# Kernel tuning notes

Measured on AMD Instinct MI355X. Metric: run time of the kernel, lower is better.

The kernel has to match this reference:

```python
import jax, jax.numpy as jnp
import numpy as np

N_BITS = 8
QMAX = 2 ** N_BITS - 1


def fake_quant(x, axis=None):
    """Min-max asymmetric uniform fake quantization with STE.
    axis=None -> per-tensor; axis=i -> per-channel along dim i."""
    if axis is None:
        mn = jnp.min(x)
        mx = jnp.max(x)
    else:
        red = tuple(i for i in range(x.ndim) if i != axis % x.ndim)
        mn = jnp.min(x, axis=red, keepdims=True)
        mx = jnp.max(x, axis=red, keepdims=True)
    mn = jnp.minimum(mn, 0.0)
    mx = jnp.maximum(mx, 0.0)
    scale = jnp.maximum((mx - mn) / QMAX, 1e-8)
    zp = jnp.round(-mn / scale)
    q = jnp.clip(jnp.round(x / scale) + zp, 0.0, QMAX)
    dq = (q - zp) * scale
    return x + jax.lax.stop_gradient(dq - x)


def setup_inputs() -> dict:
    key = jax.random.key(0)
    ks = jax.random.split(key, 5)
    B, N, C = 32, 577, 1024
    return {
        "x": jax.random.normal(ks[0], (B, N, C), dtype=jnp.float32),
        "qkv_w": jax.random.normal(ks[1], (3 * C, C), dtype=jnp.float32) * 0.02,
        "qkv_b": jax.random.normal(ks[2], (3 * C,), dtype=jnp.float32) * 0.02,
        "proj_w": jax.random.normal(ks[3], (C, C), dtype=jnp.float32) * 0.02,
        "proj_b": jax.random.normal(ks[4], (C,), dtype=jnp.float32) * 0.02,
    }


def reference(x, qkv_w, qkv_b, proj_w, proj_b):
    B, N, C = x.shape
    H = 16
    D = C // H
    scale = 1.0 / jnp.sqrt(jnp.float32(D))  # 0.125

    # QuantLinear qkv: per-channel act quant (channel_wise=True), per-out-channel weight quant
    xq = fake_quant(x, axis=-1)
    wq = fake_quant(qkv_w, axis=0)
    qkv = xq @ wq.T + qkv_b                       # [B,N,3C]
    qkv = qkv.reshape(B, N, 3, H, D).transpose(2, 0, 3, 1, 4)  # [3,B,H,N,D]
    q, k, v = qkv[0], qkv[1], qkv[2]

    # QuantMatMul 1: quantize both q and k^T (per-tensor)
    attn = jnp.einsum('bhnd,bhmd->bhnm', fake_quant(q), fake_quant(k)) * scale
    attn = jax.nn.softmax(attn, axis=-1)

    # QuantMatMul 2: disable_quantizer_a -> attn NOT quantized, only v
    out = jnp.einsum('bhnm,bhmd->bhnd', attn, fake_quant(v))  # [B,H,N,D]
    out = out.transpose(0, 2, 1, 3).reshape(B, N, C)

    # QuantLinear proj: per-tensor act quant, per-out-channel weight quant
    oq = fake_quant(out)
    pw = fake_quant(proj_w, axis=0)
    return oq @ pw.T + proj_b
```

## Files before the change

### kernel.cpp

```cpp
#include <hip/hip_runtime.h>

typedef unsigned short u16;
typedef float f32x4 __attribute__((ext_vector_type(4)));
typedef u16 u16x8 __attribute__((ext_vector_type(8)));
typedef u16 u16x4 __attribute__((ext_vector_type(4)));
typedef __bf16 bf16x8 __attribute__((ext_vector_type(8)));

#define M_ROWS 18464
#define NSEQ   577
#define NPAD   608
#define QMAXF  255.0f

static constexpr size_t OFF_IX  = 0;
static constexpr size_t OFF_BH  = 37814272;
static constexpr size_t OFF_BL  = 44105728;
static constexpr size_t OFF_IK  = 0;
static constexpr size_t OFF_IO  = 0;
static constexpr size_t OFF_F32 = 50397184;
static constexpr size_t OFF_IQ  = 50397184;
static constexpr size_t OFF_IVT = 126025728;
static constexpr size_t OFF_IPW = 165871616;
static constexpr size_t OFF_PAR = 167968768;
static constexpr size_t WS_NEED = 168100000;

#define P_XMN   0
#define P_XMX   1024
#define P_SX    2048
#define P_ZPX   3072
#define P_SWQ   4096
#define P_SPW   7168
#define P_QKVMM 8192
#define P_OUTMM 8198
#define P_PQ    8200
#define P_PO    8208

__device__ __forceinline__ u16 f2bf(float f){
  unsigned u = __float_as_uint(f);
  unsigned r = u + 0x7fffu + ((u >> 16) & 1u);
  return (u16)(r >> 16);
}
__device__ __forceinline__ float bf2f(u16 h){ return __uint_as_float(((unsigned)h) << 16); }

__device__ __forceinline__ unsigned ford(float f){
  unsigned u = __float_as_uint(f);
  return (u & 0x80000000u) ? ~u : (u | 0x80000000u);
}
__device__ __forceinline__ float unford(unsigned u){
  return (u & 0x80000000u) ? __uint_as_float(u & 0x7fffffffu) : __uint_as_float(~u);
}

__device__ __forceinline__ f32x4 mfma16(u16x8 a, u16x8 b, f32x4 c){
  return __builtin_amdgcn_mfma_f32_16x16x32_bf16(
      __builtin_bit_cast(bf16x8, a), __builtin_bit_cast(bf16x8, b), c, 0, 0, 0);
}

__device__ __forceinline__ void gload_lds16(const void* g, void* l){
  __builtin_amdgcn_global_load_lds((const __attribute__((address_space(1))) unsigned int*)g,
                                   (__attribute__((address_space(3))) unsigned int*)l,
                                   16, 0, 0);
}

__device__ __forceinline__ void tilemap(int id, int nwg, int NT, int GM, int& mt, int& nt){
  int q = nwg >> 3;
  int swz = (id & 7) * q + (id >> 3);
  int gsz = GM * NT;
  int g = swz / gsz, r = swz % gsz;
  mt = g * GM + (r % GM);
  nt = r / GM;
}

__global__ void k_init(unsigned* par){
  int t = threadIdx.x;
  for (int i = t; i < 1024; i += 256){ par[P_XMN + i] = 0xFFFFFFFFu; par[P_XMX + i] = 0u; }
  if (t < 6) par[P_QKVMM + t] = (t & 1) ? 0u : 0xFFFFFFFFu;
  if (t < 2) par[P_OUTMM + t] = (t & 1) ? 0u : 0xFFFFFFFFu;
}

__global__ void k_minmax_x(const float* __restrict__ x, unsigned* par){
  int t = threadIdx.x;
  int r0 = blockIdx.x * 145;
  int r1 = min(r0 + 145, M_ROWS);
  float mn[4], mx[4];
#pragma unroll
  for (int e = 0; e < 4; e++){ mn[e] = 1e38f; mx[e] = -1e38f; }
  for (int r = r0; r < r1; r++){
    f32x4 v = *(const f32x4*)&x[(size_t)r * 1024 + t * 4];
#pragma unroll
    for (int e = 0; e < 4; e++){ mn[e] = fminf(mn[e], v[e]); mx[e] = fmaxf(mx[e], v[e]); }
  }
#pragma unroll
  for (int e = 0; e < 4; e++){
    atomicMin(&par[P_XMN + t * 4 + e], ford(mn[e]));
    atomicMax(&par[P_XMX + t * 4 + e], ford(mx[e]));
  }
}

__global__ void k_params_x(unsigned* paru){
  float* par = (float*)paru;
  int c = blockIdx.x * 256 + threadIdx.x;
  if (c < 1024){
    float mn = unford(paru[P_XMN + c]);
    float mx = unford(paru[P_XMX + c]);
    mn = fminf(mn, 0.f); mx = fmaxf(mx, 0.f);
    float s = fmaxf((mx - mn) / QMAXF, 1e-8f);
    par[P_SX + c] = s;
    par[P_ZPX + c] = rintf(-mn / s);
  }
}

__global__ void k_quant_x(const float* __restrict__ x, const float* __restrict__ par, u16* __restrict__ ix){
  const int total = M_ROWS * 1024 / 4;
  for (int i = blockIdx.x * blockDim.x + threadIdx.x; i < total; i += gridDim.x * blockDim.x){
    f32x4 v  = *(const f32x4*)&x[(size_t)i * 4];
    int c = (i * 4) & 1023;
    f32x4 s  = *(const f32x4*)&par[P_SX + c];
    f32x4 zp = *(const f32x4*)&par[P_ZPX + c];
    u16x4 o;
#pragma unroll
    for (int e = 0; e < 4; e++){
      float q = fminf(fmaxf(rintf(v[e] / s[e]) + zp[e], 0.f), QMAXF);
      o[e] = f2bf(q - zp[e]);
    }
    *(u16x4*)&ix[(size_t)i * 4] = o;
  }
}

__global__ void k_quant_wqkv(const float* __restrict__ w, const float* __restrict__ par,
                             float* __restrict__ swq, u16* __restrict__ Bh, u16* __restrict__ Bl){
  int lane = threadIdx.x & 63, wv = threadIdx.x >> 6;
  int row = blockIdx.x * 4 + wv;
  const float* wr = w + (size_t)row * 1024;
  f32x4 v[4];
  float mn = 1e38f, mx = -1e38f;
#pragma unroll
  for (int j = 0; j < 4; j++){
    v[j] = *(const f32x4*)&wr[j * 256 + lane * 4];
#pragma unroll
    for (int e = 0; e < 4; e++){ mn = fminf(mn, v[j][e]); mx = fmaxf(mx, v[j][e]); }
  }
#pragma unroll
  for (int m = 1; m < 64; m <<= 1){ mn = fminf(mn, __shfl_xor(mn, m)); mx = fmaxf(mx, __shfl_xor(mx, m)); }
  mn = fminf(mn, 0.f); mx = fmaxf(mx, 0.f);
  float s = fmaxf((mx - mn) / QMAXF, 1e-8f);
  float zp = rintf(-mn / s);
  if (lane == 0) swq[row] = s;
#pragma unroll
  for (int j = 0; j < 4; j++){
    int c = j * 256 + lane * 4;
    f32x4 sx = *(const f32x4*)&par[P_SX + c];
    u16x4 oh, ol;
#pragma unroll
    for (int e = 0; e < 4; e++){
      float q = fminf(fmaxf(rintf(v[j][e] / s) + zp, 0.f), QMAXF);
      float bp = sx[e] * (q - zp);
      u16 hh = f2bf(bp);
      oh[e] = hh;
      ol[e] = f2bf(bp - bf2f(hh));
    }
    *(u16x4*)&Bh[(size_t)row * 1024 + c] = oh;
    *(u16x4*)&Bl[(size_t)row * 1024 + c] = ol;
  }
}

__global__ void k_quant_wproj(const float* __restrict__ w, float* __restrict__ spw, u16* __restrict__ ipw){
  int lane = threadIdx.x & 63, wv = threadIdx.x >> 6;
  int row = blockIdx.x * 4 + wv;
  const float* wr = w + (size_t)row * 1024;
  f32x4 v[4];
  float mn = 1e38f, mx = -1e38f;
#pragma unroll
  for (int j = 0; j < 4; j++){
    v[j] = *(const f32x4*)&wr[j * 256 + lane * 4];
#pragma unroll
    for (int e = 0; e < 4; e++){ mn = fminf(mn, v[j][e]); mx = fmaxf(mx, v[j][e]); }
  }
#pragma unroll
  for (int m = 1; m < 64; m <<= 1){ mn = fminf(mn, __shfl_xor(mn, m)); mx = fmaxf(mx, __shfl_xor(mx, m)); }
  mn = fminf(mn, 0.f); mx = fmaxf(mx, 0.f);
  float s = fmaxf((mx - mn) / QMAXF, 1e-8f);
  float zp = rintf(-mn / s);
  if (lane == 0) spw[row] = s;
#pragma unroll
  for (int j = 0; j < 4; j++){
    int c = j * 256 + lane * 4;
    u16x4 o;
#pragma unroll
    for (int e = 0; e < 4; e++){
      float q = fminf(fmaxf(rintf(v[j][e] / s) + zp, 0.f), QMAXF);
      o[e] = f2bf(q - zp);
    }
    *(u16x4*)&ipw[(size_t)row * 1024 + c] = o;
  }
}

__global__ __launch_bounds__(256) void k_gemm_qkvpart(const u16* __restrict__ A,
    const u16* __restrict__ Bh, const u16* __restrict__ Bl, const float* __restrict__ swq,
    const float* __restrict__ bias, int bcol_off, int NT, float* dst0, float* dst1,
    int seg0, unsigned* paru){
  __shared__ u16 As[128 * 32], Bhs[128 * 32], Bls[128 * 32];
  int tid = threadIdx.x, lane = tid & 63, w = tid >> 6;
  int mt, nt; tilemap(blockIdx.x, gridDim.x, NT, 29, mt, nt);
  int m0 = mt * 128, n0 = nt * 128;
  int wr = (w >> 1) * 64, wc = (w & 1) * 64;
  f32x4 zero = {0.f, 0.f, 0.f, 0.f};
  f32x4 acc[4][4];
#pragma unroll
  for (int m = 0; m < 4; m++)
#pragma unroll
    for (int n = 0; n < 4; n++) acc[m][n] = zero;
  int kc = (lane & 3) * 8;
  for (int kt = 0; kt < 1024; kt += 32){
    __syncthreads();
#pragma unroll
    for (int i = 0; i < 2; i++){
      int ci = w * 2 + i;
      int r = ci * 16 + (lane >> 2);
      int gra = min(m0 + r, M_ROWS - 1);
      gload_lds16(&A[(size_t)gra * 1024 + kt + kc], &As[ci * 512]);
      size_t grb = (size_t)(bcol_off + n0 + r) * 1024 + kt + kc;
      gload_lds16(&Bh[grb], &Bhs[ci * 512]);
      gload_lds16(&Bl[grb], &Bls[ci * 512]);
    }
    __syncthreads();
    u16x8 af[4];
#pragma unroll
    for (int m = 0; m < 4; m++)
      af[m] = *(const u16x8*)&As[(wr + m * 16 + (lane & 15)) * 32 + (lane >> 4) * 8];
#pragma unroll
    for (int n = 0; n < 4; n++){
      u16x8 bh = *(const u16x8*)&Bhs[(wc + n * 16 + (lane & 15)) * 32 + (lane >> 4) * 8];
      u16x8 bl = *(const u16x8*)&Bls[(wc + n * 16 + (lane & 15)) * 32 + (lane >> 4) * 8];
#pragma unroll
      for (int m = 0; m < 4; m++){
        acc[m][n] = mfma16(af[m], bh, acc[m][n]);
        acc[m][n] = mfma16(af[m], bl, acc[m][n]);
      }
    }
  }
  float lmn = 1e38f, lmx = -1e38f;
#pragma unroll
  for (int n = 0; n < 4; n++){
    int cl = n0 + wc + n * 16 + (lane & 15);
    float sw = swq[bcol_off + cl], bv = bias[bcol_off + cl];
    float* dst = (cl < 1024) ? dst0 : dst1;
    int cs = cl & 1023;
#pragma unroll
    for (int m = 0; m < 4; m++){
      int rb = m0 + wr + m * 16 + (lane >> 4) * 4;
#pragma unroll
      for (int j = 0; j < 4; j++){
        int row = rb + j;
        if (row < M_ROWS){
          float vv = acc[m][n][j] * sw + bv;
          dst[(size_t)row * 1024 + cs] = vv;
          lmn = fminf(lmn, vv); lmx = fmaxf(lmx, vv);
        }
      }
    }
  }
  int seg = seg0 + (n0 >> 10);
#pragma unroll
  for (int m = 32; m; m >>= 1){ lmn = fminf(lmn, __shfl_xor(lmn, m)); lmx = fmaxf(lmx, __shfl_xor(lmx, m)); }
  if (lane == 0){
    atomicMin(&paru[P_QKVMM + seg * 2], ford(lmn));
    atomicMax(&paru[P_QKVMM + seg * 2 + 1], ford(lmx));
  }
}

__global__ void k_params_v(unsigned* paru){
  if (threadIdx.x == 0){
    float* par = (float*)paru;
    float mn = unford(paru[P_QKVMM + 4]);
    float mx = unford(paru[P_QKVMM + 5]);
    mn = fminf(mn, 0.f); mx = fmaxf(mx, 0.f);
    float s = fmaxf((mx - mn) / QMAXF, 1e-8f);
    par[P_PQ + 4] = s;
    par[P_PQ + 5] = rintf(-mn / s);
  }
}

__global__ void k_params_qk(unsigned* paru){
  if (threadIdx.x == 0){
    float* par = (float*)paru;
    float sv[2];
    for (int t = 0; t < 2; t++){
      float mn = unford(paru[P_QKVMM + t * 2]);
      float mx = unford(paru[P_QKVMM + t * 2 + 1]);
      mn = fminf(mn, 0.f); mx = fmaxf(mx, 0.f);
      float s = fmaxf((mx - mn) / QMAXF, 1e-8f);
      sv[t] = s;
      par[P_PQ + t * 2] = s;
      par[P_PQ + t * 2 + 1] = rintf(-mn / s);
    }
    par[P_PQ + 6] = sv[0] * sv[1] * 0.125f;
  }
}

__global__ void k_quant_v(const float* __restrict__ vbuf, const float* __restrict__ par,
                          u16* __restrict__ ivT){
  int bh = blockIdx.x, b = bh >> 4, h = bh & 15;
  int tid = threadIdx.x;
  __shared__ unsigned vtu[64][37];
  float s = par[P_PQ + 4], zp = par[P_PQ + 5];
  const float* vsrc = vbuf + (size_t)b * 577 * 1024 + h * 64;
  u16* vdst = ivT + (size_t)bh * 64 * NPAD;
  for (int c0 = 0; c0 < 10; c0++){
    int n0 = c0 * 64;
    __syncthreads();
    for (int idx = tid; idx < 64 * 32; idx += 256){
      int d = idx & 63, p = idx >> 6;
      int n1 = n0 + 2 * p, n2 = n1 + 1;
      float v1 = 0.f, v2 = 0.f;
      if (n1 < NSEQ){
        float xx = vsrc[(size_t)n1 * 1024 + d];
        float q = fminf(fmaxf(rintf(xx / s) + zp, 0.f), QMAXF);
        v1 = q - zp;
      }
      if (n2 < NSEQ){
        float xx = vsrc[(size_t)n2 * 1024 + d];
        float q = fminf(fmaxf(rintf(xx / s) + zp, 0.f), QMAXF);
        v2 = q - zp;
      }
      vtu[d][p] = (unsigned)f2bf(v1) | ((unsigned)f2bf(v2) << 16);
    }
    __syncthreads();
    for (int idx = tid; idx < 64 * 32; idx += 256){
      int p = idx & 31, d = idx >> 5;
      int n = n0 + 2 * p;
      if (n < NPAD) *(unsigned*)&vdst[(size_t)d * NPAD + n] = vtu[d][p];
    }
  }
}

__global__ void k_quant_nd(const float* __restrict__ buf, const float* __restrict__ par,
                           int pidx, u16* __restrict__ dst){
  int bh = blockIdx.x, b = bh >> 4, h = bh & 15;
  int tid = threadIdx.x;
  float s = par[P_PQ + pidx], zp = par[P_PQ + pidx + 1];
  u16* d0p = dst + (size_t)bh * NPAD * 64;
  for (int idx = tid; idx < NPAD * 16; idx += 256){
    int n = idx >> 4, d0 = (idx & 15) * 4;
    u16x4 o = {0, 0, 0, 0};
    if (n < NSEQ){
      f32x4 v = *(const f32x4*)&buf[((size_t)(b * 577 + n)) * 1024 + h * 64 + d0];
#pragma unroll
      for (int e = 0; e < 4; e++){
        float q = fminf(fmaxf(rintf(v[e] / s) + zp, 0.f), QMAXF);
        o[e] = f2bf(q - zp);
      }
    }
    *(u16x4*)&d0p[n * 64 + d0] = o;
  }
}

__global__ __launch_bounds__(256) void k_attn(const u16* __restrict__ iq, const u16* __restrict__ ik,
    const u16* __restrict__ ivT, const float* __restrict__ par, float* __restrict__ out, unsigned* paru){
  __shared__ __attribute__((aligned(16))) u16 plds[4][2][2][16][40];
  int tile = blockIdx.x;
  int xcd = tile & 7, slot = tile >> 3;
  int bh = (slot / 5) * 8 + xcd, qt = slot % 5;
  int b = bh >> 4, h = bh & 15;
  int tid = threadIdx.x, lane = tid & 63, w = tid >> 6;
  int lo = lane & 15, hi = lane >> 4;
  int q0 = qt * 128 + w * 32;
  const u16* iqp = iq + (size_t)bh * NPAD * 64;
  const u16* ikp = ik + (size_t)bh * NPAD * 64;
  const u16* ivp = ivT + (size_t)bh * 64 * NPAD;
  float lscale = par[P_PQ + 6];
  u16x8 qf[2][2];
#pragma unroll
  for (int g = 0; g < 2; g++){
    int qr = min(q0 + g * 16 + lo, NPAD - 1);
#pragma unroll
    for (int ks = 0; ks < 2; ks++)
      qf[g][ks] = *(const u16x8*)&iqp[(size_t)qr * 64 + ks * 32 + hi * 8];
  }
  f32x4 zero = {0.f, 0.f, 0.f, 0.f};
  f32x4 oacc[2][4];
  float mrow[2][4], lrow[2][4];
#pragma unroll
  for (int g = 0; g < 2; g++){
#pragma unroll
    for (int n = 0; n < 4; n++) oacc[g][n] = zero;
#pragma unroll
    for (int j = 0; j < 4; j++){ mrow[g][j] = -1e30f; lrow[g][j] = 0.f; }
  }
  for (int kt = 0; kt < 19; kt++){
    int k0 = kt * 32;
    u16x8 vf[4];
#pragma unroll
    for (int n = 0; n < 4; n++)
      vf[n] = *(const u16x8*)&ivp[(size_t)(n * 16 + lo) * NPAD + k0 + hi * 8];
    u16x8 kf[2][2];
#pragma unroll
    for (int t = 0; t < 2; t++)
#pragma unroll
      for (int ks = 0; ks < 2; ks++)
        kf[t][ks] = *(const u16x8*)&ikp[(size_t)(k0 + t * 16 + lo) * 64 + ks * 32 + hi * 8];
    f32x4 acc[2][2];
#pragma unroll
    for (int g = 0; g < 2; g++)
#pragma unroll
      for (int t = 0; t < 2; t++){
        f32x4 a = mfma16(qf[g][0], kf[t][0], zero);
        acc[g][t] = mfma16(qf[g][1], kf[t][1], a);
      }
    int kg0 = k0 + lo;
#pragma unroll
    for (int g = 0; g < 2; g++){
#pragma unroll
      for (int j = 0; j < 4; j++){
        float s0 = (kg0 < NSEQ) ? acc[g][0][j] * lscale : -1e30f;
        float s1 = (kg0 + 16 < NSEQ) ? acc[g][1][j] * lscale : -1e30f;
        float mx = fmaxf(s0, s1);
#pragma unroll
        for (int mk = 1; mk < 16; mk <<= 1) mx = fmaxf(mx, __shfl_xor(mx, mk));
        float mnew = fmaxf(mrow[g][j], mx);
        float sf = __expf(mrow[g][j] - mnew);
        mrow[g][j] = mnew;
        float p0 = __expf(s0 - mnew);
        float p1 = __expf(s1 - mnew);
        float ps = p0 + p1;
#pragma unroll
        for (int mk = 1; mk < 16; mk <<= 1) ps += __shfl_xor(ps, mk);
        lrow[g][j] = lrow[g][j] * sf + ps;
#pragma unroll
        for (int n = 0; n < 4; n++) oacc[g][n][j] *= sf;
        int row = hi * 4 + j;
        u16 h0 = f2bf(p0), h1 = f2bf(p1);
        plds[w][g][0][row][lo]      = h0;
        plds[w][g][0][row][lo + 16] = h1;
        plds[w][g][1][row][lo]      = f2bf(p0 - bf2f(h0));
        plds[w][g][1][row][lo + 16] = f2bf(p1 - bf2f(h1));
      }
    }
#pragma unroll
    for (int g = 0; g < 2; g++){
      u16x8 pah = *(const u16x8*)&plds[w][g][0][lo][hi * 8];
      u16x8 pal = *(const u16x8*)&plds[w][g][1][lo][hi * 8];
#pragma unroll
      for (int n = 0; n < 4; n++){
        oacc[g][n] = mfma16(pah, vf[n], oacc[g][n]);
        oacc[g][n] = mfma16(pal, vf[n], oacc[g][n]);
      }
    }
  }
  float sv = par[P_PQ + 4];
  float lmn = 1e38f, lmx = -1e38f;
#pragma unroll
  for (int g = 0; g < 2; g++){
#pragma unroll
    for (int j = 0; j < 4; j++){
      int gn = q0 + g * 16 + hi * 4 + j;
      if (gn < NSEQ){
        float sc = sv / lrow[g][j];
#pragma unroll
        for (int n = 0; n < 4; n++){
          float vv = oacc[g][n][j] * sc;
          out[((size_t)(b * 577 + gn)) * 1024 + h * 64 + n * 16 + lo] = vv;
          lmn = fminf(lmn, vv); lmx = fmaxf(lmx, vv);
        }
      }
    }
  }
#pragma unroll
  for (int m2 = 32; m2; m2 >>= 1){ lmn = fminf(lmn, __shfl_xor(lmn, m2)); lmx = fmaxf(lmx, __shfl_xor(lmx, m2)); }
  if (lane == 0){
    atomicMin(&paru[P_OUTMM], ford(lmn));
    atomicMax(&paru[P_OUTMM + 1], ford(lmx));
  }
}

__global__ void k_params_out(unsigned* paru){
  if (threadIdx.x == 0){
    float* par = (float*)paru;
    float mn = unford(paru[P_OUTMM]), mx = unford(paru[P_OUTMM + 1]);
    mn = fminf(mn, 0.f); mx = fmaxf(mx, 0.f);
    float s = fmaxf((mx - mn) / QMAXF, 1e-8f);
    par[P_PO] = s;
    par[P_PO + 1] = rintf(-mn / s);
  }
}

__global__ void k_quant_out(const float* __restrict__ outb, const float* __restrict__ par, u16* __restrict__ io){
  float s = par[P_PO], zp = par[P_PO + 1];
  const int total = M_ROWS * 1024 / 4;
  for (int i = blockIdx.x * blockDim.x + threadIdx.x; i < total; i += gridDim.x * blockDim.x){
    f32x4 v = *(const f32x4*)&outb[(size_t)i * 4];
    u16x4 o;
#pragma unroll
    for (int e = 0; e < 4; e++){
      float q = fminf(fmaxf(rintf(v[e] / s) + zp, 0.f), QMAXF);
      o[e] = f2bf(q - zp);
    }
    *(u16x4*)&io[(size_t)i * 4] = o;
  }
}

__global__ __launch_bounds__(256) void k_gemm_proj(const u16* __restrict__ A, const u16* __restrict__ Bm,
    const float* __restrict__ spw, const float* __restrict__ par, const float* __restrict__ bias,
    float* __restrict__ Cout){
  __shared__ u16 As[128 * 32], Bs[128 * 32];
  int tid = threadIdx.x, lane = tid & 63, w = tid >> 6;
  int mt, nt; tilemap(blockIdx.x, gridDim.x, 8, 29, mt, nt);
  int m0 = mt * 128, n0 = nt * 128;
  int wr = (w >> 1) * 64, wc = (w & 1) * 64;
  f32x4 zero = {0.f, 0.f, 0.f, 0.f};
  f32x4 acc[4][4];
#pragma unroll
  for (int m = 0; m < 4; m++)
#pragma unroll
    for (int n = 0; n < 4; n++) acc[m][n] = zero;
  int kc = (lane & 3) * 8;
  for (int kt = 0; kt < 1024; kt += 32){
    __syncthreads();
#pragma unroll
    for (int i = 0; i < 2; i++){
      int ci = w * 2 + i;
      int r = ci * 16 + (lane >> 2);
      int gra = min(m0 + r, M_ROWS - 1);
      gload_lds16(&A[(size_t)gra * 1024 + kt + kc], &As[ci * 512]);
      gload_lds16(&Bm[(size_t)(n0 + r) * 1024 + kt + kc], &Bs[ci * 512]);
    }
    __syncthreads();
    u16x8 af[4];
#pragma unroll
    for (int m = 0; m < 4; m++)
      af[m] = *(const u16x8*)&As[(wr + m * 16 + (lane & 15)) * 32 + (lane >> 4) * 8];
#pragma unroll
    for (int n = 0; n < 4; n++){
      u16x8 bf = *(const u16x8*)&Bs[(wc + n * 16 + (lane & 15)) * 32 + (lane >> 4) * 8];
#pragma unroll
      for (int m = 0; m < 4; m++) acc[m][n] = mfma16(af[m], bf, acc[m][n]);
    }
  }
  float so = par[P_PO];
#pragma unroll
  for (int n = 0; n < 4; n++){
    int col = n0 + wc + n * 16 + (lane & 15);
    float sc = so * spw[col], bv = bias[col];
#pragma unroll
    for (int m = 0; m < 4; m++){
      int rb = m0 + wr + m * 16 + (lane >> 4) * 4;
#pragma unroll
      for (int j = 0; j < 4; j++){
        int row = rb + j;
        if (row < M_ROWS) Cout[(size_t)row * 1024 + col] = acc[m][n][j] * sc + bv;
      }
    }
  }
}

extern "C" void kernel_launch(void* const* d_in, const int* in_sizes, int n_in,
                              void* d_out, int out_size, void* d_ws, size_t ws_size,
                              hipStream_t stream){
  (void)in_sizes; (void)n_in; (void)out_size;
  if (ws_size < WS_NEED) return;
  const float* x      = (const float*)d_in[0];
  const float* qkv_w  = (const float*)d_in[1];
  const float* qkv_b  = (const float*)d_in[2];
  const float* proj_w = (const float*)d_in[3];
  const float* proj_b = (const float*)d_in[4];
  char* ws = (char*)d_ws;
  u16*   ix   = (u16*)(ws + OFF_IX);
  u16*   Bh   = (u16*)(ws + OFF_BH);
  u16*   Bl   = (u16*)(ws + OFF_BL);
  u16*   ik   = (u16*)(ws + OFF_IK);
  u16*   io   = (u16*)(ws + OFF_IO);
  float* f32b = (float*)(ws + OFF_F32);
  u16*   iq   = (u16*)(ws + OFF_IQ);
  u16*   ivT  = (u16*)(ws + OFF_IVT);
  u16*   ipw  = (u16*)(ws + OFF_IPW);
  unsigned* paru = (unsigned*)(ws + OFF_PAR);
  float* parf = (float*)paru;
  float* qbuf = (float*)d_out;

  k_init<<<1, 256, 0, stream>>>(paru);
  k_minmax_x<<<128, 256, 0, stream>>>(x, paru);
  k_params_x<<<4, 256, 0, stream>>>(paru);
  k_quant_x<<<1024, 256, 0, stream>>>(x, parf, ix);
  k_quant_wqkv<<<768, 256, 0, stream>>>(qkv_w, parf, parf + P_SWQ, Bh, Bl);
  k_quant_wproj<<<256, 256, 0, stream>>>(proj_w, parf + P_SPW, ipw);
  k_gemm_qkvpart<<<1160, 256, 0, stream>>>(ix, Bh, Bl, parf + P_SWQ, qkv_b, 2048, 8, f32b, f32b, 2, paru);
  k_params_v<<<1, 64, 0, stream>>>(paru);
  k_quant_v<<<512, 256, 0, stream>>>(f32b, parf, ivT);
  k_gemm_qkvpart<<<2320, 256, 0, stream>>>(ix, Bh, Bl, parf + P_SWQ, qkv_b, 0, 16, qbuf, f32b, 0, paru);
  k_params_qk<<<1, 64, 0, stream>>>(paru);
  k_quant_nd<<<512, 256, 0, stream>>>(f32b, parf, 2, ik);
  k_quant_nd<<<512, 256, 0, stream>>>(qbuf, parf, 0, iq);
  k_attn<<<2560, 256, 0, stream>>>(iq, ik, ivT, parf, (float*)d_out, paru);
  k_params_out<<<1, 64, 0, stream>>>(paru);
  k_quant_out<<<1024, 256, 0, stream>>>((float*)d_out, parf, io);
  k_gemm_proj<<<1160, 256, 0, stream>>>(io, ipw, parf + P_SPW, parf, proj_b, (float*)d_out);
}
```

Before: 1.237 ms.

## Replace online softmax max with Cauchy-Schwarz row bound precomputed in quant

When K is quantized, the kernel now records the global maximum squared norm of the quantized K rows. When Q is quantized, it computes a per-row upper bound lscale*|q|*max|k| and stores it. The attention kernel uses this fixed bound as the softmax shift, removing the per-tile max shuffles, rescale exponentials and accumulator rescaling, and reduces the row sum only once at the end. The risk is underflow: if the bound far exceeds the true row max, exp values become tiny and bf16 precision suffers, though scores here are small enough that this is likely tolerable.

```diff
diff --git a/kernel.cpp b/kernel.cpp
--- a/kernel.cpp
+++ b/kernel.cpp
@@ -16,6 +16,7 @@
 static constexpr size_t OFF_BL  = 44105728;
 static constexpr size_t OFF_IK  = 0;
 static constexpr size_t OFF_IO  = 0;
+static constexpr size_t OFF_ROWM= 39845888;
 static constexpr size_t OFF_F32 = 50397184;
 static constexpr size_t OFF_IQ  = 50397184;
 static constexpr size_t OFF_IVT = 126025728;
@@ -33,6 +34,7 @@
 #define P_OUTMM 8198
 #define P_PQ    8200
 #define P_PO    8208
+#define P_KN2   8210
 
 __device__ __forceinline__ u16 f2bf(float f){
   unsigned u = __float_as_uint(f);
@@ -74,6 +76,7 @@
   for (int i = t; i < 1024; i += 256){ par[P_XMN + i] = 0xFFFFFFFFu; par[P_XMX + i] = 0u; }
   if (t < 6) par[P_QKVMM + t] = (t & 1) ? 0u : 0xFFFFFFFFu;
   if (t < 2) par[P_OUTMM + t] = (t & 1) ? 0u : 0xFFFFFFFFu;
+  if (t == 0) par[P_KN2] = 0u;
 }
 
 __global__ void k_minmax_x(const float* __restrict__ x, unsigned* par){
@@ -333,28 +336,48 @@
 }
 
 __global__ void k_quant_nd(const float* __restrict__ buf, const float* __restrict__ par,
-                           int pidx, u16* __restrict__ dst){
+                           int pidx, u16* __restrict__ dst, float* __restrict__ rowm,
+                           unsigned* paru){
   int bh = blockIdx.x, b = bh >> 4, h = bh & 15;
   int tid = threadIdx.x;
   float s = par[P_PQ + pidx], zp = par[P_PQ + pidx + 1];
+  float lscale = par[P_PQ + 6];
+  float kn2 = (pidx == 0) ? unford(paru[P_KN2]) : 0.f;
   u16* d0p = dst + (size_t)bh * NPAD * 64;
+  float kmx = 0.f;
   for (int idx = tid; idx < NPAD * 16; idx += 256){
     int n = idx >> 4, d0 = (idx & 15) * 4;
     u16x4 o = {0, 0, 0, 0};
+    float s2 = 0.f;
     if (n < NSEQ){
       f32x4 v = *(const f32x4*)&buf[((size_t)(b * 577 + n)) * 1024 + h * 64 + d0];
 #pragma unroll
       for (int e = 0; e < 4; e++){
         float q = fminf(fmaxf(rintf(v[e] / s) + zp, 0.f), QMAXF);
-        o[e] = f2bf(q - zp);
+        float a = q - zp;
+        o[e] = f2bf(a);
+        s2 += a * a;
       }
     }
     *(u16x4*)&d0p[n * 64 + d0] = o;
+    s2 += __shfl_xor(s2, 1); s2 += __shfl_xor(s2, 2);
+    s2 += __shfl_xor(s2, 4); s2 += __shfl_xor(s2, 8);
+    if (pidx == 2){
+      kmx = fmaxf(kmx, s2);
+    } else if ((tid & 15) == 0){
+      rowm[(size_t)bh * NPAD + n] = lscale * sqrtf(s2 * kn2);
+    }
+  }
+  if (pidx == 2){
+    kmx = fmaxf(kmx, __shfl_xor(kmx, 16));
+    kmx = fmaxf(kmx, __shfl_xor(kmx, 32));
+    if ((tid & 63) == 0) atomicMax(&paru[P_KN2], ford(kmx));
   }
 }
 
 __global__ __launch_bounds__(256) void k_attn(const u16* __restrict__ iq, const u16* __restrict__ ik,
-    const u16* __restrict__ ivT, const float* __restrict__ par, float* __restrict__ out, unsigned* paru){
+    const u16* __restrict__ ivT, const float* __restrict__ rowm, const float* __restrict__ par,
+    float* __restrict__ out, unsigned* paru){
   __shared__ __attribute__((aligned(16))) u16 plds[4][2][2][16][40];
   int tile = blockIdx.x;
   int xcd = tile & 7, slot = tile >> 3;
@@ -366,24 +389,29 @@
   const u16* iqp = iq + (size_t)bh * NPAD * 64;
   const u16* ikp = ik + (size_t)bh * NPAD * 64;
   const u16* ivp = ivT + (size_t)bh * 64 * NPAD;
+  const float* rowmp = rowm + (size_t)bh * NPAD;
   float lscale = par[P_PQ + 6];
   u16x8 qf[2][2];
+  float Mg[2][4];
 #pragma unroll
   for (int g = 0; g < 2; g++){
     int qr = min(q0 + g * 16 + lo, NPAD - 1);
 #pragma unroll
     for (int ks = 0; ks < 2; ks++)
       qf[g][ks] = *(const u16x8*)&iqp[(size_t)qr * 64 + ks * 32 + hi * 8];
+#pragma unroll
+    for (int j = 0; j < 4; j++)
+      Mg[g][j] = rowmp[min(q0 + g * 16 + hi * 4 + j, NPAD - 1)];
   }
   f32x4 zero = {0.f, 0.f, 0.f, 0.f};
   f32x4 oacc[2][4];
-  float mrow[2][4], lrow[2][4];
+  float lrow[2][4];
 #pragma unroll
   for (int g = 0; g < 2; g++){
 #pragma unroll
     for (int n = 0; n < 4; n++) oacc[g][n] = zero;
 #pragma unroll
-    for (int j = 0; j < 4; j++){ mrow[g][j] = -1e30f; lrow[g][j] = 0.f; }
+    for (int j = 0; j < 4; j++) lrow[g][j] = 0.f;
   }
   for (int kt = 0; kt < 19; kt++){
     int k0 = kt * 32;
@@ -412,20 +440,9 @@
       for (int j = 0; j < 4; j++){
         float s0 = (kg0 < NSEQ) ? acc[g][0][j] * lscale : -1e30f;
         float s1 = (kg0 + 16 < NSEQ) ? acc[g][1][j] * lscale : -1e30f;
-        float mx = fmaxf(s0, s1);
-#pragma unroll
-        for (int mk = 1; mk < 16; mk <<= 1) mx = fmaxf(mx, __shfl_xor(mx, mk));
-        float mnew = fmaxf(mrow[g][j], mx);
-        float sf = __expf(mrow[g][j] - mnew);
-        mrow[g][j] = mnew;
-        float p0 = __expf(s0 - mnew);
-        float p1 = __expf(s1 - mnew);
-        float ps = p0 + p1;
-#pragma unroll
-        for (int mk = 1; mk < 16; mk <<= 1) ps += __shfl_xor(ps, mk);
-        lrow[g][j] = lrow[g][j] * sf + ps;
-#pragma unroll
-        for (int n = 0; n < 4; n++) oacc[g][n][j] *= sf;
+        float p0 = __expf(s0 - Mg[g][j]);
+        float p1 = __expf(s1 - Mg[g][j]);
+        lrow[g][j] += p0 + p1;
         int row = hi * 4 + j;
         u16 h0 = f2bf(p0), h1 = f2bf(p1);
         plds[w][g][0][row][lo]      = h0;
@@ -445,6 +462,15 @@
       }
     }
   }
+#pragma unroll
+  for (int g = 0; g < 2; g++)
+#pragma unroll
+    for (int j = 0; j < 4; j++){
+      float l = lrow[g][j];
+      l += __shfl_xor(l, 1); l += __shfl_xor(l, 2);
+      l += __shfl_xor(l, 4); l += __shfl_xor(l, 8);
+      lrow[g][j] = l;
+    }
   float sv = par[P_PQ + 4];
   float lmn = 1e38f, lmx = -1e38f;
 #pragma unroll
@@ -567,6 +593,7 @@
   u16*   Bl   = (u16*)(ws + OFF_BL);
   u16*   ik   = (u16*)(ws + OFF_IK);
   u16*   io   = (u16*)(ws + OFF_IO);
+  float* rowm = (float*)(ws + OFF_ROWM);
   float* f32b = (float*)(ws + OFF_F32);
   u16*   iq   = (u16*)(ws + OFF_IQ);
   u16*   ivT  = (u16*)(ws + OFF_IVT);
@@ -586,9 +613,9 @@
   k_quant_v<<<512, 256, 0, stream>>>(f32b, parf, ivT);
   k_gemm_qkvpart<<<2320, 256, 0, stream>>>(ix, Bh, Bl, parf + P_SWQ, qkv_b, 0, 16, qbuf, f32b, 0, paru);
   k_params_qk<<<1, 64, 0, stream>>>(paru);
-  k_quant_nd<<<512, 256, 0, stream>>>(f32b, parf, 2, ik);
-  k_quant_nd<<<512, 256, 0, stream>>>(qbuf, parf, 0, iq);
-  k_attn<<<2560, 256, 0, stream>>>(iq, ik, ivT, parf, (float*)d_out, paru);
+  k_quant_nd<<<512, 256, 0, stream>>>(f32b, parf, 2, ik, rowm, paru);
+  k_quant_nd<<<512, 256, 0, stream>>>(qbuf, parf, 0, iq, rowm, paru);
+  k_attn<<<2560, 256, 0, stream>>>(iq, ik, ivT, rowm, parf, (float*)d_out, paru);
   k_params_out<<<1, 64, 0, stream>>>(paru);
   k_quant_out<<<1024, 256, 0, stream>>>((float*)d_out, parf, io);
   k_gemm_proj<<<1160, 256, 0, stream>>>(io, ipw, parf + P_SPW, parf, proj_b, (float*)d_out);
```

New measurement: 1.281 ms. 3.6% more time.
